# Performance work log

Hardware: AMD Instinct MI355X
Metric: run time of the kernel (lower is better)

Reference implementation:

```python
import jax, jax.numpy as jnp
import numpy as np
from jax import lax

H = 512      # hidden_size (== embed dim)
K = 128      # attr_size
V = 32000    # output_size (vocab)
ANUM = 20    # aspect_num = len(aspect_ids)//100
N, B = 64, 32
T, S, A = 256, 32, 5


def setup_inputs() -> dict:
    key = jax.random.key(0)
    ks = jax.random.split(key, 32)
    f = lambda i, shape, s=0.02: (jax.random.normal(ks[i], shape, jnp.float32) * s)
    inp = {
        "input_seq": jax.random.randint(ks[0], (N, B), 0, V, jnp.int32),
        "last_hidden": jax.random.normal(ks[1], (1, B, H), jnp.float32),
        "encoder_out1": jax.random.normal(ks[2], (T, B, H), jnp.float32),
        "encoder_out2": jax.random.normal(ks[3], (S, B, H), jnp.float32),
        "encoder_out3": jax.random.normal(ks[4], (A, B, K), jnp.float32),
        "encoder_out4": jax.random.normal(ks[5], (A, B, ANUM), jnp.float32),
        "aspect_ids": jax.random.randint(ks[6], (100 * ANUM,), 0, V, jnp.int32),
        # learned parameters
        "emb": f(7, (V, H)),
        "gru_Wih": f(8, (3 * H, H)), "gru_Whh": f(9, (3 * H, H)),
        "gru_bih": f(10, (3 * H,)), "gru_bhh": f(11, (3 * H,)),
        "attn_W": f(12, (H, 2 * H)), "attn_b": f(13, (H,)), "attn_v": f(14, (H,)),
        "attr_W": f(15, (H, H + K)), "attr_b": f(16, (H,)), "attr_v": f(17, (H,)),
        "concat_W": f(18, (H, 3 * H + K)), "concat_b": f(19, (H,)),
        "out_W": f(20, (V, H)), "out_b": f(21, (V,)),
        "gate_W": f(22, (ANUM, 2 * H + ANUM)), "gate_b": f(23, (ANUM,)),
        "proj_W": f(24, (ANUM, 2 * ANUM)), "proj_b": f(25, (ANUM,)),
    }
    return inp


def _gru(x, h0, Wih, Whh, bih, bhh):
    # x: (N,B,H); h0: (B,H). PyTorch gate order: reset, update, new.
    def step(h, xt):
        gi = xt @ Wih.T + bih
        gh = h @ Whh.T + bhh
        ir, iz, inn = jnp.split(gi, 3, axis=-1)
        hr, hz, hn = jnp.split(gh, 3, axis=-1)
        r = jax.nn.sigmoid(ir + hr)
        z = jax.nn.sigmoid(iz + hz)
        n = jnp.tanh(inn + r * hn)
        h_new = (1.0 - z) * n + z * h
        return h_new, h_new
    hT, ys = lax.scan(step, h0, x)
    return ys, hT


def _attn(hidden, enc, W, b, v):
    # Faithful to Attn/AttributeAttn: energies[b,n,t] = tanh(v . (W @ cat(hidden[n,b], enc[t,b]) + b))
    # W @ cat = hidden @ Wh^T + enc @ We^T; dot with v distributes -> avoid (T,N,B,*) blowup.
    Hh = hidden.shape[-1]
    Wh, We = W[:, :Hh], W[:, Hh:]
    a = hidden @ (Wh.T @ v) + jnp.dot(b, v)   # (N,B)
    c = enc @ (We.T @ v)                       # (T,B)
    e = jnp.tanh(a.T[:, :, None] + c.T[:, None, :])  # (B,N,T)
    return jax.nn.softmax(e, axis=2)


def reference(input_seq, last_hidden, encoder_out1, encoder_out2, encoder_out3,
              encoder_out4, aspect_ids, emb, gru_Wih, gru_Whh, gru_bih, gru_bhh,
              attn_W, attn_b, attn_v, attr_W, attr_b, attr_v, concat_W, concat_b,
              out_W, out_b, gate_W, gate_b, proj_W, proj_b):
    seq_len = input_seq.shape[0]
    embedded = emb[input_seq]                                   # (N,B,H), dropout=eval noop
    rnn_output, hT = _gru(embedded, last_hidden[0], gru_Wih, gru_Whh, gru_bih, gru_bhh)
    hidden = hT[None]                                           # (1,B,H)

    aw1 = _attn(rnn_output, encoder_out1, attn_W, attn_b, attn_v)   # (B,N,T)
    ctx1 = jnp.einsum('bnt,tbh->nbh', aw1, encoder_out1)
    aw2 = _attn(rnn_output, encoder_out2, attn_W, attn_b, attn_v)   # (B,N,S)
    ctx2 = jnp.einsum('bns,sbh->nbh', aw2, encoder_out2)
    aw3 = _attn(rnn_output, encoder_out3, attr_W, attr_b, attr_v)   # (B,N,A)
    ctx3 = jnp.einsum('bna,abk->nbk', aw3, encoder_out3)

    concat_input = jnp.concatenate([rnn_output, ctx1, ctx2, ctx3], axis=2)
    concat_output = jnp.tanh(concat_input @ concat_W.T + concat_b)  # (N,B,H)
    output = concat_output @ out_W.T + out_b                        # (N,B,V)

    e4 = jnp.concatenate([encoder_out4[0], encoder_out4[1]], axis=-1)  # (B,2*ANUM)
    e4 = e4 @ proj_W.T + proj_b                                        # (B,ANUM)
    e4 = jnp.broadcast_to(e4[None], (seq_len,) + e4.shape)             # (N,B,ANUM)

    gate = jnp.tanh(jnp.concatenate([embedded, rnn_output, e4], axis=2) @ gate_W.T + gate_b)
    vals = jnp.tile(gate, (1, 1, 100))                                 # (N,B,100*ANUM)
    output = output.at[:, :, aspect_ids].add(vals)
    return output, hidden, aw1, aw2, aw3, gate
```

## Files before the change

kernel.cpp:

```cpp
#include <hip/hip_runtime.h>
#include <hip/hip_bf16.h>

#define HDIM 512
#define KA   128
#define VOC  32000
#define ANUMC 20
#define NSEQ 64
#define BATCH 32
#define TLEN 256
#define SLEN 32
#define ALEN 5
#define NB   2048
#define CIN  1664
#define G3H  1536
#define GB   64

typedef __bf16 bf16;
typedef bf16 v8bf __attribute__((ext_vector_type(8)));
typedef float v4f __attribute__((ext_vector_type(4)));

#define DEV __device__ __forceinline__

DEV float sigmoidf_(float x) { return 1.f / (1.f + expf(-x)); }

__global__ void k_zero(int* bar) {
  for (int i = threadIdx.x; i < GB * 32; i += 256) bar[i] = 0;
}

__global__ void k_vec(const float* __restrict__ attn_W, const float* __restrict__ attn_b,
                      const float* __restrict__ attn_v,
                      const float* __restrict__ attr_W, const float* __restrict__ attr_b,
                      const float* __restrict__ attr_v,
                      const float* __restrict__ enc4, const float* __restrict__ pW,
                      const float* __restrict__ pb, float* __restrict__ misc) {
  int tid = threadIdx.x;
  int blk = blockIdx.x;
  if (blk == 0) {
    for (int i = tid; i < 512; i += 256) {
      float s = 0.f;
      for (int j = 0; j < 512; ++j) s += attn_W[j * 1024 + i] * attn_v[j];
      misc[i] = s;
    }
  } else if (blk == 1) {
    for (int i = tid; i < 512; i += 256) {
      float s = 0.f;
      for (int j = 0; j < 512; ++j) s += attn_W[j * 1024 + 512 + i] * attn_v[j];
      misc[512 + i] = s;
    }
  } else if (blk == 2) {
    for (int i = tid; i < 512; i += 256) {
      float s = 0.f;
      for (int j = 0; j < 512; ++j) s += attr_W[j * 640 + i] * attr_v[j];
      misc[1024 + i] = s;
    }
  } else {
    for (int i = tid; i < 128; i += 256) {
      float s = 0.f;
      for (int j = 0; j < 512; ++j) s += attr_W[j * 640 + 512 + i] * attr_v[j];
      misc[1536 + i] = s;
    }
    if (tid == 128) {
      float s = 0.f;
      for (int j = 0; j < 512; ++j) s += attn_b[j] * attn_v[j];
      misc[1664] = s;
    }
    if (tid == 129) {
      float s = 0.f;
      for (int j = 0; j < 512; ++j) s += attr_b[j] * attr_v[j];
      misc[1665] = s;
    }
    for (int i = tid; i < BATCH * ANUMC; i += 256) {
      int b = i / ANUMC, j = i % ANUMC;
      float s = pb[j];
      for (int q = 0; q < ANUMC; ++q) s += pW[j * 40 + q] * enc4[b * ANUMC + q];
      for (int q = 0; q < ANUMC; ++q) s += pW[j * 40 + 20 + q] * enc4[BATCH * ANUMC + b * ANUMC + q];
      misc[1792 + i] = s;
    }
  }
}

__global__ void k_embcvt(const int* __restrict__ seq, const float* __restrict__ emb,
                         float* __restrict__ embedded, bf16* __restrict__ emb_bf,
                         const float* __restrict__ Wih, bf16* __restrict__ Wih_bf,
                         const float* __restrict__ cW, bf16* __restrict__ cW_bf,
                         const float* __restrict__ oW, bf16* __restrict__ oW_bf) {
  size_t i = (size_t)blockIdx.x * 256 + threadIdx.x;
  const size_t s0 = 1048576, s1 = s0 + 786432, s2 = s1 + 851968, s3 = s2 + 16384000;
  if (i < s0) {
    int row = (int)(i >> 9), col = (int)(i & 511);
    float v = emb[(size_t)seq[row] * 512 + col];
    embedded[i] = v;
    emb_bf[i] = (bf16)v;
  } else if (i < s1) {
    size_t j = i - s0;
    Wih_bf[j] = (bf16)Wih[j];
  } else if (i < s2) {
    size_t j = i - s1;
    cW_bf[j] = (bf16)cW[j];
  } else if (i < s3) {
    size_t j = i - s2;
    oW_bf[j] = (bf16)oW[j];
  }
}

__global__ void k_c(const float* __restrict__ enc1, const float* __restrict__ enc2,
                    const float* __restrict__ enc3, float* __restrict__ misc) {
  int i = blockIdx.x * 256 + threadIdx.x;
  const float* u1e = misc + 512;
  const float* u3e = misc + 1536;
  if (i < 8192) {
    const float* row = enc1 + (size_t)i * 512;
    float s = 0.f;
#pragma unroll 4
    for (int j = 0; j < 512; j += 4) {
      float4 a = *(const float4*)(row + j);
      float4 u = *(const float4*)(u1e + j);
      s += a.x * u.x + a.y * u.y + a.z * u.z + a.w * u.w;
    }
    misc[2560 + i] = s;
  } else if (i < 8192 + 1024) {
    int k = i - 8192;
    const float* row = enc2 + (size_t)k * 512;
    float s = 0.f;
#pragma unroll 4
    for (int j = 0; j < 512; j += 4) {
      float4 a = *(const float4*)(row + j);
      float4 u = *(const float4*)(u1e + j);
      s += a.x * u.x + a.y * u.y + a.z * u.z + a.w * u.w;
    }
    misc[10752 + k] = s;
  } else if (i < 8192 + 1024 + 160) {
    int k = i - 9216;
    const float* row = enc3 + (size_t)k * 128;
    float s = 0.f;
#pragma unroll 4
    for (int j = 0; j < 128; j += 4) {
      float4 a = *(const float4*)(row + j);
      float4 u = *(const float4*)(u3e + j);
      s += a.x * u.x + a.y * u.y + a.z * u.z + a.w * u.w;
    }
    misc[11776 + k] = s;
  }
}

template <int EPI>
__global__ __launch_bounds__(256) void k_gemm_bt(const bf16* __restrict__ A,
                                                 const bf16* __restrict__ Bm,
                                                 const float* __restrict__ bias,
                                                 float* __restrict__ Cf, bf16* __restrict__ Cb,
                                                 int M, int Nn, int Kd) {
  __shared__ __align__(16) unsigned short As[128 * 64];
  __shared__ __align__(16) unsigned short Bs[128 * 64];
  int tid = threadIdx.x;
  int m0 = blockIdx.y * 128;
  int n0 = blockIdx.x * 128;
  int lane = tid & 63;
  int wv = tid >> 6;
  int wm = wv & 1, wn = wv >> 1;
  int l15 = lane & 15, quad = lane >> 4;
  int srow = tid >> 3;
  int sch = tid & 7;

  v4f acc[4][4];
#pragma unroll
  for (int i = 0; i < 4; ++i)
#pragma unroll
    for (int j = 0; j < 4; ++j) acc[i][j] = (v4f){0.f, 0.f, 0.f, 0.f};

  for (int kb = 0; kb < Kd; kb += 64) {
#pragma unroll
    for (int r = 0; r < 4; ++r) {
      int row = r * 32 + srow;
      uint4 va = *(const uint4*)(A + (size_t)(m0 + row) * Kd + kb + sch * 8);
      *(uint4*)((char*)As + row * 128 + ((sch ^ (row & 7)) << 4)) = va;
      uint4 vb = *(const uint4*)(Bm + (size_t)(n0 + row) * Kd + kb + sch * 8);
      *(uint4*)((char*)Bs + row * 128 + ((sch ^ (row & 7)) << 4)) = vb;
    }
    __syncthreads();
#pragma unroll
    for (int ks = 0; ks < 2; ++ks) {
      v8bf af[4], bfr[4];
      int c = ks * 4 + quad;
#pragma unroll
      for (int i = 0; i < 4; ++i) {
        int mr = wm * 64 + i * 16 + l15;
        af[i] = *(const v8bf*)((const char*)As + mr * 128 + ((c ^ (mr & 7)) << 4));
      }
#pragma unroll
      for (int j = 0; j < 4; ++j) {
        int nr = wn * 64 + j * 16 + l15;
        bfr[j] = *(const v8bf*)((const char*)Bs + nr * 128 + ((c ^ (nr & 7)) << 4));
      }
#pragma unroll
      for (int i = 0; i < 4; ++i)
#pragma unroll
        for (int j = 0; j < 4; ++j)
          acc[i][j] = __builtin_amdgcn_mfma_f32_16x16x32_bf16(af[i], bfr[j], acc[i][j], 0, 0, 0);
    }
    __syncthreads();
  }
#pragma unroll
  for (int i = 0; i < 4; ++i) {
    int gr0 = m0 + wm * 64 + i * 16 + quad * 4;
#pragma unroll
    for (int j = 0; j < 4; ++j) {
      int gc = n0 + wn * 64 + j * 16 + l15;
      float bs = bias[gc];
#pragma unroll
      for (int reg = 0; reg < 4; ++reg) {
        float v = acc[i][j][reg] + bs;
        if (EPI == 1)
          Cb[(size_t)(gr0 + reg) * Nn + gc] = (bf16)tanhf(v);
        else
          Cf[(size_t)(gr0 + reg) * Nn + gc] = v;
      }
    }
  }
}

__global__ __launch_bounds__(256) void k_gru(const float* __restrict__ gi,
                                             const float* __restrict__ Whh,
                                             const float* __restrict__ bhh,
                                             const float* __restrict__ lasth,
                                             float* __restrict__ rnn,
                                             bf16* __restrict__ concat_bf,
                                             bf16* __restrict__ h_x,
                                             int* __restrict__ bar) {
  struct SMEM {
    unsigned short whh[24 * 512];
    unsigned short hs[32 * 512];
    float gh[32 * 29];
    unsigned short hnew[256];
  };
  __shared__ __align__(16) SMEM sm;
  int tid = threadIdx.x;
  int blk = blockIdx.x;
  int c0 = blk * 8;

  for (int idx = tid; idx < 24 * 64; idx += 256) {
    int row = idx >> 6, cc = idx & 63;
    int g = row >> 3, jj = row & 7;
    const float* src = Whh + (size_t)(g * 512 + c0 + jj) * 512 + cc * 8;
    float4 x = *(const float4*)src;
    float4 y = *(const float4*)(src + 4);
    v8bf vv;
    vv[0] = (bf16)x.x; vv[1] = (bf16)x.y; vv[2] = (bf16)x.z; vv[3] = (bf16)x.w;
    vv[4] = (bf16)y.x; vv[5] = (bf16)y.y; vv[6] = (bf16)y.z; vv[7] = (bf16)y.w;
    *(v8bf*)((char*)sm.whh + row * 1024 + ((cc ^ (row & 7)) << 4)) = vv;
  }

  int lane = tid & 63;
  int w = tid >> 6;
  int l15 = lane & 15, quad = lane >> 4;
  int m0 = (w & 1) * 16;
  int n0 = (w >> 1) * 16;

  int cb = tid >> 3, j = tid & 7, c = c0 + j;
  float hprev = lasth[cb * 512 + c];
  float b_r = bhh[c], b_z = bhh[512 + c], b_n = bhh[1024 + c];

  for (int t = 0; t < 64; ++t) {
    const float* gii = gi + ((size_t)t * 32 + cb) * G3H;
    float g_r = gii[c];
    float g_z = gii[512 + c];
    float g_n = gii[1024 + c];

    if (t == 0) {
#pragma unroll
      for (int rnd = 0; rnd < 8; ++rnd) {
        int ch = rnd * 256 + tid;
        int bb = ch >> 6, cc = ch & 63;
        const float* hp = lasth + bb * 512 + cc * 8;
        float4 x = *(const float4*)hp;
        float4 y = *(const float4*)(hp + 4);
        v8bf vv;
        vv[0] = (bf16)x.x; vv[1] = (bf16)x.y; vv[2] = (bf16)x.z; vv[3] = (bf16)x.w;
        vv[4] = (bf16)y.x; vv[5] = (bf16)y.y; vv[6] = (bf16)y.z; vv[7] = (bf16)y.w;
        *(v8bf*)((char*)sm.hs + bb * 1024 + ((cc ^ (bb & 7)) << 4)) = vv;
      }
    } else {
#pragma unroll
      for (int rnd = 0; rnd < 8; ++rnd) {
        int ch = rnd * 256 + tid;
        int bb = ch >> 6, cc = ch & 63;
        const unsigned long long* src = (const unsigned long long*)(h_x + bb * 512 + cc * 8);
        unsigned long long a0 = __hip_atomic_load(src, __ATOMIC_RELAXED, __HIP_MEMORY_SCOPE_AGENT);
        unsigned long long a1 = __hip_atomic_load(src + 1, __ATOMIC_RELAXED, __HIP_MEMORY_SCOPE_AGENT);
        uint4 v;
        v.x = (unsigned)a0; v.y = (unsigned)(a0 >> 32);
        v.z = (unsigned)a1; v.w = (unsigned)(a1 >> 32);
        *(uint4*)((char*)sm.hs + bb * 1024 + ((cc ^ (bb & 7)) << 4)) = v;
      }
    }
    __syncthreads();

    {
      v4f acc = (v4f){0.f, 0.f, 0.f, 0.f};
#pragma unroll
      for (int it = 0; it < 16; ++it) {
        int cc = it * 4 + quad;
        int mr = m0 + l15;
        v8bf af = *(const v8bf*)((const char*)sm.hs + mr * 1024 + ((cc ^ (mr & 7)) << 4));
        int nr = n0 + l15;
        v8bf bfr = *(const v8bf*)((const char*)sm.whh + nr * 1024 + ((cc ^ (nr & 7)) << 4));
        acc = __builtin_amdgcn_mfma_f32_16x16x32_bf16(af, bfr, acc, 0, 0, 0);
      }
      if (n0 == 0 || l15 < 8) {
#pragma unroll
        for (int reg = 0; reg < 4; ++reg)
          sm.gh[(m0 + quad * 4 + reg) * 29 + n0 + l15] = acc[reg];
      }
    }
    __syncthreads();

    {
      float ar = sm.gh[cb * 29 + j] + b_r;
      float az = sm.gh[cb * 29 + 8 + j] + b_z;
      float an = sm.gh[cb * 29 + 16 + j] + b_n;
      float rg = sigmoidf_(g_r + ar);
      float zg = sigmoidf_(g_z + az);
      float ng = tanhf(g_n + rg * an);
      float hn = (1.f - zg) * ng + zg * hprev;
      hprev = hn;
      rnn[((size_t)t * 32 + cb) * 512 + c] = hn;
      bf16 hb = (bf16)hn;
      concat_bf[((size_t)t * 32 + cb) * CIN + c] = hb;
      sm.hnew[tid] = *(unsigned short*)&hb;
    }

    if (t < 63) {
      __syncthreads();
      if (tid < 64) {
        int q = tid;
        int cbq = q >> 1, j0 = (q & 1) * 4;
        const unsigned short* hp = sm.hnew + q * 4;
        unsigned long long pk = (unsigned long long)hp[0] | ((unsigned long long)hp[1] << 16) |
                                ((unsigned long long)hp[2] << 32) |
                                ((unsigned long long)hp[3] << 48);
        __hip_atomic_store((unsigned long long*)(h_x + cbq * 512 + c0 + j0), pk,
                           __ATOMIC_RELAXED, __HIP_MEMORY_SCOPE_AGENT);
      }
      __syncthreads();
      if (tid == 0)
        __hip_atomic_store(&bar[blk * 32], t + 1, __ATOMIC_RELAXED, __HIP_MEMORY_SCOPE_AGENT);
      if (w == 0) {
        int target = t + 1;
        for (;;) {
          int v = __hip_atomic_load(&bar[lane * 32], __ATOMIC_RELAXED, __HIP_MEMORY_SCOPE_AGENT);
          if (__all(v >= target)) break;
          __builtin_amdgcn_s_sleep(1);
        }
      }
      __atomic_signal_fence(__ATOMIC_SEQ_CST);
      __syncthreads();
    }
  }
}

__global__ __launch_bounds__(256) void k_attnrow(const float* __restrict__ rnn,
                                                 const float* __restrict__ misc,
                                                 float* __restrict__ aw1,
                                                 float* __restrict__ aw2,
                                                 float* __restrict__ aw3) {
  int wv = (blockIdx.x * 256 + threadIdx.x) >> 6;
  int lane = threadIdx.x & 63;
  if (wv >= 2048) return;
  int n = wv >> 5, b = wv & 31;
  const float* u1a = misc;
  const float* u3h = misc + 1024;
  const float* c1 = misc + 2560;
  const float* c2 = misc + 10752;
  const float* c3 = misc + 11776;
  const float* row = rnn + (size_t)(n * 32 + b) * 512;
  float s1 = 0.f, s3 = 0.f;
#pragma unroll
  for (int q = 0; q < 8; ++q) {
    int j = lane * 8 + q;
    float rv = row[j];
    s1 += rv * u1a[j];
    s3 += rv * u3h[j];
  }
  for (int o = 32; o > 0; o >>= 1) {
    s1 += __shfl_down(s1, o);
    s3 += __shfl_down(s3, o);
  }
  s1 = __shfl(s1, 0) + misc[1664];
  s3 = __shfl(s3, 0) + misc[1665];

  float e[4];
  float mx = -1e30f;
#pragma unroll
  for (int q = 0; q < 4; ++q) {
    int t = q * 64 + lane;
    e[q] = tanhf(s1 + c1[t * 32 + b]);
    mx = fmaxf(mx, e[q]);
  }
  for (int o = 32; o > 0; o >>= 1) mx = fmaxf(mx, __shfl_xor(mx, o));
  float sum = 0.f;
#pragma unroll
  for (int q = 0; q < 4; ++q) {
    e[q] = expf(e[q] - mx);
    sum += e[q];
  }
  for (int o = 32; o > 0; o >>= 1) sum += __shfl_xor(sum, o);
  float inv = 1.f / sum;
  size_t base1 = (size_t)(b * 64 + n) * 256;
#pragma unroll
  for (int q = 0; q < 4; ++q) aw1[base1 + q * 64 + lane] = e[q] * inv;

  float e2 = (lane < 32) ? tanhf(s1 + c2[lane * 32 + b]) : -1e30f;
  float m2 = e2;
  for (int o = 32; o > 0; o >>= 1) m2 = fmaxf(m2, __shfl_xor(m2, o));
  float x2 = (lane < 32) ? expf(e2 - m2) : 0.f;
  float sm2 = x2;
  for (int o = 32; o > 0; o >>= 1) sm2 += __shfl_xor(sm2, o);
  if (lane < 32) aw2[(size_t)(b * 64 + n) * 32 + lane] = x2 / sm2;

  float e3 = (lane < 5) ? tanhf(s3 + c3[lane * 32 + b]) : -1e30f;
  float m3 = e3;
  for (int o = 32; o > 0; o >>= 1) m3 = fmaxf(m3, __shfl_xor(m3, o));
  float x3 = (lane < 5) ? expf(e3 - m3) : 0.f;
  float sm3 = x3;
  for (int o = 32; o > 0; o >>= 1) sm3 += __shfl_xor(sm3, o);
  if (lane < 5) aw3[(size_t)(b * 64 + n) * 5 + lane] = x3 / sm3;
}

template <int TL, int COFF>
__global__ __launch_bounds__(256) void k_ctx(const float* __restrict__ aw,
                                             const float* __restrict__ enc,
                                             bf16* __restrict__ concat_bf) {
  __shared__ __align__(16) float awsT[TL * 36];
  int tid = threadIdx.x;
  int bx = blockIdx.x;
  int b = bx >> 2, q = (bx >> 1) & 1, nh = bx & 1;
  for (int i = tid; i < 32 * TL; i += 256) {
    int n = i / TL, te = i % TL;
    awsT[te * 36 + n] = aw[(size_t)b * 64 * TL + (size_t)(nh * 32 + n) * TL + te];
  }
  __syncthreads();
  int col = q * 256 + tid;
  float4 acc[8];
#pragma unroll
  for (int n4 = 0; n4 < 8; ++n4) acc[n4] = make_float4(0.f, 0.f, 0.f, 0.f);
  for (int te = 0; te < TL; ++te) {
    float v = enc[((size_t)te * 32 + b) * 512 + col];
#pragma unroll
    for (int n4 = 0; n4 < 8; ++n4) {
      float4 wv = *(const float4*)(awsT + te * 36 + n4 * 4);
      acc[n4].x += wv.x * v;
      acc[n4].y += wv.y * v;
      acc[n4].z += wv.z * v;
      acc[n4].w += wv.w * v;
    }
  }
#pragma unroll
  for (int n4 = 0; n4 < 8; ++n4) {
    int ng = nh * 32 + n4 * 4;
    concat_bf[((size_t)(ng + 0) * 32 + b) * CIN + COFF + col] = (bf16)acc[n4].x;
    concat_bf[((size_t)(ng + 1) * 32 + b) * CIN + COFF + col] = (bf16)acc[n4].y;
    concat_bf[((size_t)(ng + 2) * 32 + b) * CIN + COFF + col] = (bf16)acc[n4].z;
    concat_bf[((size_t)(ng + 3) * 32 + b) * CIN + COFF + col] = (bf16)acc[n4].w;
  }
}

__global__ void k_ctx3_misc(const float* __restrict__ aw3, const float* __restrict__ enc3,
                            const float* __restrict__ rnn, bf16* __restrict__ concat_bf,
                            float* __restrict__ hid) {
  int i = blockIdx.x * 256 + threadIdx.x;
  if (i < NB * 128) {
    int row = i >> 7, k = i & 127;
    int n = row >> 5, b = row & 31;
    float s = 0.f;
#pragma unroll
    for (int a = 0; a < 5; ++a)
      s += aw3[(size_t)(b * 64 + n) * 5 + a] * enc3[((size_t)a * 32 + b) * 128 + k];
    concat_bf[(size_t)row * CIN + 1536 + k] = (bf16)s;
  } else {
    int j = i - NB * 128;
    if (j < 16384) hid[j] = rnn[(size_t)63 * 16384 + j];
  }
}

__global__ __launch_bounds__(256) void k_gate(const float* __restrict__ embedded,
                                              const float* __restrict__ rnn,
                                              const float* __restrict__ misc,
                                              const float* __restrict__ gW,
                                              const float* __restrict__ gb,
                                              float* __restrict__ gate) {
  int i = blockIdx.x * 256 + threadIdx.x;
  if (i >= NB * ANUMC) return;
  int row = i / ANUMC, j = i % ANUMC;
  int b = row & 31;
  const float* w = gW + (size_t)j * 1044;
  const float* e = embedded + (size_t)row * 512;
  const float* r = rnn + (size_t)row * 512;
  float s = gb[j];
#pragma unroll 4
  for (int k = 0; k < 512; k += 4) {
    float4 a = *(const float4*)(e + k);
    float4 ww = *(const float4*)(w + k);
    s += a.x * ww.x + a.y * ww.y + a.z * ww.z + a.w * ww.w;
  }
#pragma unroll 4
  for (int k = 0; k < 512; k += 4) {
    float4 a = *(const float4*)(r + k);
    float4 ww = *(const float4*)(w + 512 + k);
    s += a.x * ww.x + a.y * ww.y + a.z * ww.z + a.w * ww.w;
  }
  const float* e4 = misc + 1792 + b * ANUMC;
#pragma unroll
  for (int q = 0; q < ANUMC; ++q) s += w[1024 + q] * e4[q];
  gate[i] = tanhf(s);
}

__global__ __launch_bounds__(256) void k_aspect(const int* __restrict__ ids,
                                                const float* __restrict__ gate,
                                                float* __restrict__ out) {
  __shared__ float gs[ANUMC];
  int row = blockIdx.x;
  if (threadIdx.x < ANUMC) gs[threadIdx.x] = gate[(size_t)row * ANUMC + threadIdx.x];
  __syncthreads();
  float* orow = out + (size_t)row * VOC;
  for (int k = threadIdx.x; k < 2000; k += 256) {
    atomicAdd(orow + ids[k], gs[k % ANUMC]);
  }
}

extern "C" void kernel_launch(void* const* d_in, const int* in_sizes, int n_in,
                              void* d_out, int out_size, void* d_ws, size_t ws_size,
                              hipStream_t stream) {
  const int* seq = (const int*)d_in[0];
  const float* lasth = (const float*)d_in[1];
  const float* enc1 = (const float*)d_in[2];
  const float* enc2 = (const float*)d_in[3];
  const float* enc3 = (const float*)d_in[4];
  const float* enc4 = (const float*)d_in[5];
  const int* aspect = (const int*)d_in[6];
  const float* emb = (const float*)d_in[7];
  const float* Wih = (const float*)d_in[8];
  const float* Whh = (const float*)d_in[9];
  const float* bih = (const float*)d_in[10];
  const float* bhh = (const float*)d_in[11];
  const float* attn_W = (const float*)d_in[12];
  const float* attn_b = (const float*)d_in[13];
  const float* attn_v = (const float*)d_in[14];
  const float* attr_W = (const float*)d_in[15];
  const float* attr_b = (const float*)d_in[16];
  const float* attr_v = (const float*)d_in[17];
  const float* cW = (const float*)d_in[18];
  const float* cbias = (const float*)d_in[19];
  const float* oW = (const float*)d_in[20];
  const float* ob = (const float*)d_in[21];
  const float* gW = (const float*)d_in[22];
  const float* gb = (const float*)d_in[23];
  const float* pW = (const float*)d_in[24];
  const float* pb = (const float*)d_in[25];

  char* ws = (char*)d_ws;
  float* misc = (float*)(ws + 0);
  float* embedded = (float*)(ws + 65536);
  float* gi = (float*)(ws + 4259840);
  float* rnn = (float*)(ws + 16842752);
  bf16* emb_bf = (bf16*)(ws + 21037056);
  bf16* Wih_bf = (bf16*)(ws + 23134208);
  bf16* cW_bf = (bf16*)(ws + 24707072);
  bf16* oW_bf = (bf16*)(ws + 26411008);
  bf16* concat_bf = (bf16*)(ws + 59179008);
  bf16* cout_bf = (bf16*)(ws + 65994752);
  bf16* h_x = (bf16*)(ws + 68091904);
  int* bar = (int*)(misc + 12032);

  float* out = (float*)d_out;
  float* hid_out = out + 65536000;
  float* aw1 = out + 65552384;
  float* aw2 = out + 66076672;
  float* aw3 = out + 66142208;
  float* gate = out + 66152448;

  k_zero<<<1, 256, 0, stream>>>(bar);
  k_vec<<<4, 256, 0, stream>>>(attn_W, attn_b, attn_v, attr_W, attr_b, attr_v, enc4, pW, pb, misc);
  k_embcvt<<<74496, 256, 0, stream>>>(seq, emb, embedded, emb_bf, Wih, Wih_bf, cW, cW_bf, oW,
                                      oW_bf);
  k_c<<<37, 256, 0, stream>>>(enc1, enc2, enc3, misc);
  k_gemm_bt<0><<<dim3(12, 16), 256, 0, stream>>>(emb_bf, Wih_bf, bih, gi, nullptr, NB, G3H, 512);
  k_gru<<<GB, 256, 0, stream>>>(gi, Whh, bhh, lasth, rnn, concat_bf, h_x, bar);
  k_attnrow<<<512, 256, 0, stream>>>(rnn, misc, aw1, aw2, aw3);
  k_ctx<256, 512><<<128, 256, 0, stream>>>(aw1, enc1, concat_bf);
  k_ctx<32, 1024><<<128, 256, 0, stream>>>(aw2, enc2, concat_bf);
  k_ctx3_misc<<<1088, 256, 0, stream>>>(aw3, enc3, rnn, concat_bf, hid_out);
  k_gate<<<160, 256, 0, stream>>>(embedded, rnn, misc, gW, gb, gate);
  k_gemm_bt<1><<<dim3(4, 16), 256, 0, stream>>>(concat_bf, cW_bf, cbias, nullptr, cout_bf, NB,
                                                512, CIN);
  k_gemm_bt<0><<<dim3(250, 16), 256, 0, stream>>>(cout_bf, oW_bf, ob, out, nullptr, NB, VOC, 512);
  k_aspect<<<2048, 256, 0, stream>>>(aspect, gate, out);
}
```

Baseline: 1.208 ms.

## Replace GRU grid barrier with tagged double-buffered hidden-state exchange

The per-step grid barrier in the persistent GRU kernel (flag store plus a spin over all block flags) is removed. Each 64-bit slot now carries two bf16 hidden values and a 32-bit tag built from a per-launch counter and the step index. Readers spin only until every slot they need has the current tag, using two double-buffered slots to avoid overwrite races. The Whh MFMA loop is also split into two independent accumulators to expose more ILP. The cost is more global atomic traffic, since each thread polls 32 slots, and correctness now rests on the tag protocol and the counter-increment kernel.

```diff
diff --git a/kernel.cpp b/kernel.cpp
--- a/kernel.cpp
+++ b/kernel.cpp
@@ -23,8 +23,8 @@
 
 DEV float sigmoidf_(float x) { return 1.f / (1.f + expf(-x)); }
 
-__global__ void k_zero(int* bar) {
-  for (int i = threadIdx.x; i < GB * 32; i += 256) bar[i] = 0;
+__global__ void k_tick(unsigned* ctr) {
+  if (threadIdx.x == 0) ++*ctr;
 }
 
 __global__ void k_vec(const float* __restrict__ attn_W, const float* __restrict__ attn_b,
@@ -224,8 +224,8 @@
                                              const float* __restrict__ lasth,
                                              float* __restrict__ rnn,
                                              bf16* __restrict__ concat_bf,
-                                             bf16* __restrict__ h_x,
-                                             int* __restrict__ bar) {
+                                             unsigned long long* __restrict__ hx,
+                                             const unsigned* __restrict__ ctr) {
   struct SMEM {
     unsigned short whh[24 * 512];
     unsigned short hs[32 * 512];
@@ -236,6 +236,7 @@
   int tid = threadIdx.x;
   int blk = blockIdx.x;
   int c0 = blk * 8;
+  unsigned tagbase = (*ctr) << 6;
 
   for (int idx = tid; idx < 24 * 64; idx += 256) {
     int row = idx >> 6, cc = idx & 63;
@@ -279,32 +280,52 @@
         *(v8bf*)((char*)sm.hs + bb * 1024 + ((cc ^ (bb & 7)) << 4)) = vv;
       }
     } else {
-#pragma unroll
-      for (int rnd = 0; rnd < 8; ++rnd) {
-        int ch = rnd * 256 + tid;
-        int bb = ch >> 6, cc = ch & 63;
-        const unsigned long long* src = (const unsigned long long*)(h_x + bb * 512 + cc * 8);
-        unsigned long long a0 = __hip_atomic_load(src, __ATOMIC_RELAXED, __HIP_MEMORY_SCOPE_AGENT);
-        unsigned long long a1 = __hip_atomic_load(src + 1, __ATOMIC_RELAXED, __HIP_MEMORY_SCOPE_AGENT);
-        uint4 v;
-        v.x = (unsigned)a0; v.y = (unsigned)(a0 >> 32);
-        v.z = (unsigned)a1; v.w = (unsigned)(a1 >> 32);
-        *(uint4*)((char*)sm.hs + bb * 1024 + ((cc ^ (bb & 7)) << 4)) = v;
-      }
+      unsigned tg = tagbase + (unsigned)t;
+      const unsigned long long* src = hx + (size_t)(t & 1) * 8192 + tid;
+      unsigned long long v[32];
+#pragma unroll
+      for (int i = 0; i < 32; ++i)
+        v[i] = __hip_atomic_load(src + i * 256, __ATOMIC_RELAXED, __HIP_MEMORY_SCOPE_AGENT);
+      for (;;) {
+        unsigned stale = 0u;
+#pragma unroll
+        for (int i = 0; i < 32; ++i)
+          if ((unsigned)(v[i] >> 32) != tg) stale |= (1u << i);
+        if (!stale) break;
+        __builtin_amdgcn_s_sleep(1);
+#pragma unroll
+        for (int i = 0; i < 32; ++i)
+          if (stale & (1u << i))
+            v[i] = __hip_atomic_load(src + i * 256, __ATOMIC_RELAXED, __HIP_MEMORY_SCOPE_AGENT);
+      }
+      int cc = tid >> 2, b4 = (tid & 3) * 4;
+#pragma unroll
+      for (int i = 0; i < 32; ++i)
+        *(unsigned*)((char*)sm.hs + i * 1024 + (((cc ^ (i & 7)) << 4) | b4)) = (unsigned)v[i];
     }
     __syncthreads();
 
     {
-      v4f acc = (v4f){0.f, 0.f, 0.f, 0.f};
-#pragma unroll
-      for (int it = 0; it < 16; ++it) {
-        int cc = it * 4 + quad;
-        int mr = m0 + l15;
-        v8bf af = *(const v8bf*)((const char*)sm.hs + mr * 1024 + ((cc ^ (mr & 7)) << 4));
-        int nr = n0 + l15;
-        v8bf bfr = *(const v8bf*)((const char*)sm.whh + nr * 1024 + ((cc ^ (nr & 7)) << 4));
-        acc = __builtin_amdgcn_mfma_f32_16x16x32_bf16(af, bfr, acc, 0, 0, 0);
-      }
+      v4f acc0 = (v4f){0.f, 0.f, 0.f, 0.f};
+      v4f acc1 = (v4f){0.f, 0.f, 0.f, 0.f};
+      int mr = m0 + l15;
+      int nr = n0 + l15;
+#pragma unroll
+      for (int it = 0; it < 8; ++it) {
+        {
+          int ccx = it * 4 + quad;
+          v8bf af = *(const v8bf*)((const char*)sm.hs + mr * 1024 + ((ccx ^ (mr & 7)) << 4));
+          v8bf bfr = *(const v8bf*)((const char*)sm.whh + nr * 1024 + ((ccx ^ (nr & 7)) << 4));
+          acc0 = __builtin_amdgcn_mfma_f32_16x16x32_bf16(af, bfr, acc0, 0, 0, 0);
+        }
+        {
+          int ccx = (it + 8) * 4 + quad;
+          v8bf af = *(const v8bf*)((const char*)sm.hs + mr * 1024 + ((ccx ^ (mr & 7)) << 4));
+          v8bf bfr = *(const v8bf*)((const char*)sm.whh + nr * 1024 + ((ccx ^ (nr & 7)) << 4));
+          acc1 = __builtin_amdgcn_mfma_f32_16x16x32_bf16(af, bfr, acc1, 0, 0, 0);
+        }
+      }
+      v4f acc = acc0 + acc1;
       if (n0 == 0 || l15 < 8) {
 #pragma unroll
         for (int reg = 0; reg < 4; ++reg)
@@ -330,29 +351,15 @@
 
     if (t < 63) {
       __syncthreads();
-      if (tid < 64) {
-        int q = tid;
-        int cbq = q >> 1, j0 = (q & 1) * 4;
-        const unsigned short* hp = sm.hnew + q * 4;
-        unsigned long long pk = (unsigned long long)hp[0] | ((unsigned long long)hp[1] << 16) |
-                                ((unsigned long long)hp[2] << 32) |
-                                ((unsigned long long)hp[3] << 48);
-        __hip_atomic_store((unsigned long long*)(h_x + cbq * 512 + c0 + j0), pk,
+      if (tid < 128) {
+        int cbq = tid >> 2, wj = tid & 3;
+        const unsigned short* hp = sm.hnew + cbq * 8 + wj * 2;
+        unsigned long long pk = (unsigned long long)hp[0] |
+                                ((unsigned long long)hp[1] << 16) |
+                                ((unsigned long long)(tagbase + (unsigned)(t + 1)) << 32);
+        __hip_atomic_store(hx + (size_t)((t + 1) & 1) * 8192 + cbq * 256 + blk * 4 + wj, pk,
                            __ATOMIC_RELAXED, __HIP_MEMORY_SCOPE_AGENT);
       }
-      __syncthreads();
-      if (tid == 0)
-        __hip_atomic_store(&bar[blk * 32], t + 1, __ATOMIC_RELAXED, __HIP_MEMORY_SCOPE_AGENT);
-      if (w == 0) {
-        int target = t + 1;
-        for (;;) {
-          int v = __hip_atomic_load(&bar[lane * 32], __ATOMIC_RELAXED, __HIP_MEMORY_SCOPE_AGENT);
-          if (__all(v >= target)) break;
-          __builtin_amdgcn_s_sleep(1);
-        }
-      }
-      __atomic_signal_fence(__ATOMIC_SEQ_CST);
-      __syncthreads();
     }
   }
 }
@@ -567,8 +574,8 @@
   bf16* oW_bf = (bf16*)(ws + 26411008);
   bf16* concat_bf = (bf16*)(ws + 59179008);
   bf16* cout_bf = (bf16*)(ws + 65994752);
-  bf16* h_x = (bf16*)(ws + 68091904);
-  int* bar = (int*)(misc + 12032);
+  unsigned long long* hx = (unsigned long long*)(ws + 68091904);
+  unsigned* ctr = (unsigned*)(misc + 12032);
 
   float* out = (float*)d_out;
   float* hid_out = out + 65536000;
@@ -577,13 +584,13 @@
   float* aw3 = out + 66142208;
   float* gate = out + 66152448;
 
-  k_zero<<<1, 256, 0, stream>>>(bar);
+  k_tick<<<1, 64, 0, stream>>>(ctr);
   k_vec<<<4, 256, 0, stream>>>(attn_W, attn_b, attn_v, attr_W, attr_b, attr_v, enc4, pW, pb, misc);
   k_embcvt<<<74496, 256, 0, stream>>>(seq, emb, embedded, emb_bf, Wih, Wih_bf, cW, cW_bf, oW,
                                       oW_bf);
   k_c<<<37, 256, 0, stream>>>(enc1, enc2, enc3, misc);
   k_gemm_bt<0><<<dim3(12, 16), 256, 0, stream>>>(emb_bf, Wih_bf, bih, gi, nullptr, NB, G3H, 512);
-  k_gru<<<GB, 256, 0, stream>>>(gi, Whh, bhh, lasth, rnn, concat_bf, h_x, bar);
+  k_gru<<<GB, 256, 0, stream>>>(gi, Whh, bhh, lasth, rnn, concat_bf, hx, ctr);
   k_attnrow<<<512, 256, 0, stream>>>(rnn, misc, aw1, aw2, aw3);
   k_ctx<256, 512><<<128, 256, 0, stream>>>(aw1, enc1, concat_bf);
   k_ctx<32, 1024><<<128, 256, 0, stream>>>(aw2, enc2, concat_bf);
```

Measured after the change: 1.232 ms. Within noise of the previous version (+2.0%).
